# Performance work log

Hardware: AMD Instinct MI355X
Metric: run time of the kernel (lower is better)

## Reference

```python
import jax, jax.numpy as jnp
import numpy as np
import math
from jax import lax

IMG = 1024
STRIDES = (4, 8, 16, 32, 64)
RATIOS = (0.5, 1.0, 2.0)
PRE_NMS = 1000      # pre_nms_top_n['testing'] per level
POST_NMS = 1000     # post_nms_top_n['testing']
NMS_T = 0.7
MIN_SIZE = 1e-3
SCORE_T = 0.0
BBOX_CLAMP = math.log(1000.0 / 16.0)  # torchvision BoxCoder clamp
LEVEL_SIZES = tuple(((IMG // s) ** 2) * len(RATIOS) for s in STRIDES)  # (196608,49152,12288,3072,768)
A_TOTAL = sum(LEVEL_SIZES)
N_IMG = 16


def _make_anchors():
    ratios = np.asarray(RATIOS, dtype=np.float64)
    h_r = np.sqrt(ratios)
    w_r = 1.0 / h_r
    out = []
    for lvl, s in enumerate(STRIDES):
        size = 32.0 * (2 ** lvl)
        ws, hs = w_r * size, h_r * size
        base = np.stack([-ws / 2, -hs / 2, ws / 2, hs / 2], axis=1)  # [A,4]
        g = IMG // s
        coords = np.arange(g, dtype=np.float64) * s
        sx, sy = np.meshgrid(coords, coords)  # [g,g], row = H
        shifts = np.stack([sx, sy, sx, sy], axis=-1).reshape(-1, 1, 4)  # [g*g,1,4] in (H,W,A) order
        out.append((shifts + base[None]).reshape(-1, 4))
    return np.concatenate(out, 0).astype(np.float32)


def setup_inputs() -> dict:
    key = jax.random.key(0)
    k1, k2 = jax.random.split(key)
    objectness = jax.random.normal(k1, (N_IMG, A_TOTAL), dtype=jnp.float32)
    deltas = jax.random.normal(k2, (N_IMG, A_TOTAL, 4), dtype=jnp.float32) * 0.1
    anchors = jnp.asarray(_make_anchors())
    return {"objectness": objectness, "deltas": deltas, "anchors": anchors}


def _decode(deltas, anchors):
    # torchvision BoxCoder.decode with weights (1,1,1,1); deltas [N,A,4], anchors [A,4]
    wa = anchors[:, 2] - anchors[:, 0]
    ha = anchors[:, 3] - anchors[:, 1]
    cxa = anchors[:, 0] + 0.5 * wa
    cya = anchors[:, 1] + 0.5 * ha
    dx, dy, dw, dh = (deltas[..., 0], deltas[..., 1], deltas[..., 2], deltas[..., 3])
    dw = jnp.minimum(dw, BBOX_CLAMP)
    dh = jnp.minimum(dh, BBOX_CLAMP)
    cx = dx * wa + cxa
    cy = dy * ha + cya
    w = jnp.exp(dw) * wa
    h = jnp.exp(dh) * ha
    return jnp.stack([cx - 0.5 * w, cy - 0.5 * h, cx + 0.5 * w, cy + 0.5 * h], axis=-1)


def _nms_image(boxes, scores, lvl, valid):
    # batched_nms via per-level coordinate offset, then greedy NMS over score-sorted boxes.
    max_c = jnp.max(boxes)
    off = lvl.astype(boxes.dtype) * (max_c + 1.0)
    b_off = boxes + off[:, None]
    s = jnp.where(valid, scores, -1.0)
    order = jnp.argsort(-s)
    b = b_off[order]          # [K,4] offset boxes, score-descending
    bo = boxes[order]
    so = scores[order]
    vo = valid[order]
    K = b.shape[0]
    areas = (b[:, 2] - b[:, 0]) * (b[:, 3] - b[:, 1])
    idx = jnp.arange(K)

    def body(keep, xs):
        i, bi, vi = xs
        lt = jnp.maximum(bi[:2], b[:, :2])
        rb = jnp.minimum(bi[2:], b[:, 2:])
        wh = jnp.clip(rb - lt, 0.0)
        inter = wh[:, 0] * wh[:, 1]
        ai = (bi[2] - bi[0]) * (bi[3] - bi[1])
        union = ai + areas - inter
        iou = jnp.where(union > 0, inter / union, 0.0)
        suppressed = jnp.any(keep & (idx < i) & (iou > NMS_T))
        return keep.at[i].set(vi & ~suppressed), None

    keep, _ = lax.scan(body, jnp.zeros((K,), bool), (idx, b, vo))
    # compact kept entries (already score-ordered) into POST_NMS slots, pad with zeros
    pos = jnp.cumsum(keep) - 1
    slot = jnp.where(keep & (pos < POST_NMS), pos, POST_NMS)
    out_b = jnp.zeros((POST_NMS + 1, 4), boxes.dtype).at[slot].set(bo)[:POST_NMS]
    out_s = jnp.zeros((POST_NMS + 1,), boxes.dtype).at[slot].set(so)[:POST_NMS]
    return out_b, out_s


def reference(objectness, deltas, anchors):
    N = objectness.shape[0]
    proposals = _decode(deltas, anchors)  # [N,A,4]
    # per-level top-k (pre-NMS)
    idxs = []
    offset = 0
    for n in LEVEL_SIZES:
        k = min(PRE_NMS, n)
        _, ti = lax.top_k(objectness[:, offset:offset + n], k)
        idxs.append(ti + offset)
        offset += n
    top_idx = jnp.concatenate(idxs, axis=1)  # [N,K]
    obj = jnp.take_along_axis(objectness, top_idx, axis=1)
    props = jnp.take_along_axis(proposals, top_idx[..., None], axis=1)
    lvl_full = jnp.asarray(np.repeat(np.arange(len(LEVEL_SIZES)), LEVEL_SIZES))
    lvl = lvl_full[top_idx]
    scores = jax.nn.sigmoid(obj)
    # clip to image
    x = jnp.clip(props[..., 0::2], 0.0, float(IMG))
    y = jnp.clip(props[..., 1::2], 0.0, float(IMG))
    boxes = jnp.stack([x[..., 0], y[..., 0], x[..., 1], y[..., 1]], axis=-1)
    # remove small boxes + score threshold (as validity mask)
    w = boxes[..., 2] - boxes[..., 0]
    h = boxes[..., 3] - boxes[..., 1]
    valid = (w >= MIN_SIZE) & (h >= MIN_SIZE) & (scores >= SCORE_T)
    out_boxes, out_scores = jax.vmap(_nms_image)(boxes, scores, lvl, valid)
    return out_boxes, out_scores
```

## Files before the change

kernel.cpp:

```cpp
#include <hip/hip_runtime.h>
#include <stdint.h>

#define NIMG 16
#define ATOT 261888
#define TOTC 4768
#define POSTN 1000
#define ROWQ 75
#define EQCAP 8192
#define SCAP 1088
#define BPRE 24
#define DM 0.7000000178813934326171875

__device__ __forceinline__ unsigned sortable_u32(float f) {
  unsigned b = __float_as_uint(f);
  return (b & 0x80000000u) ? ~b : (b | 0x80000000u);
}

__device__ __forceinline__ float exp_xla(float x) {
  float xc = fminf(x, 88.72283935546875f);
  xc = fmaxf(xc, -87.33654022216796875f);
  float n = floorf(fmaf(xc, 1.44269504088896341f, 0.5f));
  float r = fmaf(n, -0.693359375f, xc);
  r = fmaf(n, 2.12194440e-4f, r);
  float y = 1.9875691500e-4f;
  y = fmaf(y, r, 1.3981999507e-3f);
  y = fmaf(y, r, 8.3334519073e-3f);
  y = fmaf(y, r, 4.1665795894e-2f);
  y = fmaf(y, r, 1.6666665459e-1f);
  y = fmaf(y, r, 5.0000001201e-1f);
  float r2 = r * r;
  y = fmaf(y, r2, r);
  y = y + 1.0f;
  return ldexpf(y, (int)n);
}

__device__ __forceinline__ float sigmoid_ref(float x) {
#pragma clang fp contract(off)
  float e = exp_xla(-x);
  return 1.0f / (1.0f + e);
}

__device__ __forceinline__ void chunk_map4k(int c, int& lvl, int& start, int& cnt) {
  if (c < 48)      { lvl = 0; start = c * 4096;        cnt = 4096; }
  else if (c < 60) { lvl = 1; start = (c - 48) * 4096; cnt = 4096; }
  else if (c < 63) { lvl = 2; start = (c - 60) * 4096; cnt = 4096; }
  else             { lvl = 3; start = 0;               cnt = 3072; }
}
__constant__ int d_LO[5] = {0, 196608, 245760, 258048, 261120};
__constant__ int d_CO[5] = {0, 1000, 2000, 3000, 4000};

__global__ void __launch_bounds__(256) k_hist(const float* __restrict__ obj,
                                              unsigned* __restrict__ hist) {
  int img = blockIdx.x >> 6, c = blockIdx.x & 63;
  int lvl, start, cnt;
  chunk_map4k(c, lvl, start, cnt);
  const float4* p4 = (const float4*)(obj + (size_t)img * ATOT + d_LO[lvl] + start);
  __shared__ unsigned h[256];
  h[threadIdx.x] = 0;
  __syncthreads();
  int nv = cnt >> 2;
  for (int i = threadIdx.x; i < nv; i += 256) {
    float4 v = p4[i];
    atomicAdd(&h[sortable_u32(v.x) >> 24], 1u);
    atomicAdd(&h[sortable_u32(v.y) >> 24], 1u);
    atomicAdd(&h[sortable_u32(v.z) >> 24], 1u);
    atomicAdd(&h[sortable_u32(v.w) >> 24], 1u);
  }
  __syncthreads();
  unsigned* gh = hist + (img * 4 + lvl) * 256;
  if (h[threadIdx.x]) atomicAdd(&gh[threadIdx.x], h[threadIdx.x]);
}

__global__ void __launch_bounds__(64) k_thresh(const unsigned* __restrict__ hist,
                                               unsigned* __restrict__ thr) {
  int il = blockIdx.x;
  if (threadIdx.x != 0) return;
  const unsigned* h = hist + il * 256;
  unsigned krem = 1000, cum = 0;
  int d = 255;
  for (; d > 0; --d) {
    if (cum + h[d] >= krem) break;
    cum += h[d];
  }
  thr[il * 2] = (unsigned)d;
  thr[il * 2 + 1] = krem - cum;
}

__global__ void __launch_bounds__(256) k_emit(const float* __restrict__ obj,
                                              const unsigned* __restrict__ thr,
                                              int* __restrict__ cand,
                                              int* __restrict__ eqbuf,
                                              unsigned* __restrict__ cnt) {
  int img = blockIdx.x / 65, c = blockIdx.x % 65;
  if (c == 64) {
    for (int i = threadIdx.x; i < 768; i += 256)
      cand[img * TOTC + d_CO[4] + i] = d_LO[4] + i;
    return;
  }
  int lvl, start, cntn;
  chunk_map4k(c, lvl, start, cntn);
  int il = img * 4 + lvl;
  unsigned d0 = thr[il * 2];
  int gbase = d_LO[lvl] + start;
  const float4* p4 = (const float4*)(obj + (size_t)img * ATOT + gbase);
  int nv = cntn >> 2;
  int cbase = img * TOTC + d_CO[lvl];

  __shared__ int gts[SCAP], eqs[SCAP];
  __shared__ int nGt, nEq, gtBase, eqBase;
  if (threadIdx.x == 0) { nGt = 0; nEq = 0; }
  __syncthreads();

  float4 v[4];
  int ni = 0;
#pragma unroll
  for (int k = 0; k < 4; ++k) {
    int i = threadIdx.x + k * 256;
    if (i < nv) { v[k] = p4[i]; ni = k + 1; }
  }
#pragma unroll
  for (int k = 0; k < 4; ++k) {
    if (k >= ni) break;
    float vv[4] = {v[k].x, v[k].y, v[k].z, v[k].w};
#pragma unroll
    for (int c4 = 0; c4 < 4; ++c4) {
      unsigned u = sortable_u32(vv[c4]);
      unsigned d = u >> 24;
      if (d >= d0) {
        int gidx = gbase + (threadIdx.x + k * 256) * 4 + c4;
        if (d > d0) {
          int p = atomicAdd(&nGt, 1);
          if (p < SCAP) gts[p] = gidx;
          else { int s = (int)atomicAdd(&cnt[il * 2], 1u); cand[cbase + s] = gidx; }
        } else {
          int p = atomicAdd(&nEq, 1);
          if (p < SCAP) eqs[p] = gidx;
          else { int e = (int)atomicAdd(&cnt[il * 2 + 1], 1u); if (e < EQCAP) eqbuf[il * EQCAP + e] = gidx; }
        }
      }
    }
  }
  __syncthreads();
  int ng = nGt < SCAP ? nGt : SCAP;
  int ne = nEq < SCAP ? nEq : SCAP;
  if (threadIdx.x == 0) {
    gtBase = (int)atomicAdd(&cnt[il * 2], (unsigned)ng);
    eqBase = (int)atomicAdd(&cnt[il * 2 + 1], (unsigned)ne);
  }
  __syncthreads();
  for (int k = threadIdx.x; k < ng; k += 256) cand[cbase + gtBase + k] = gts[k];
  for (int k = threadIdx.x; k < ne; k += 256) {
    int e = eqBase + k;
    if (e < EQCAP) eqbuf[il * EQCAP + e] = eqs[k];
  }
}

__global__ void __launch_bounds__(256) k_refine(const float* __restrict__ obj,
                                                const unsigned* __restrict__ thr,
                                                const int* __restrict__ eqbuf,
                                                const unsigned* __restrict__ cnt,
                                                int* __restrict__ cand) {
  int il = blockIdx.x;
  int img = il >> 2, lvl = il & 3;
  unsigned pref = thr[il * 2];
  unsigned krem = thr[il * 2 + 1];
  int neq = min((int)cnt[il * 2 + 1], EQCAP);
  int cgt = (int)cnt[il * 2];
  const float* p = obj + (size_t)img * ATOT;
  const int* eq = eqbuf + il * EQCAP;
  int cbase = img * TOTC + d_CO[lvl];
  __shared__ unsigned h[256];
  __shared__ unsigned s_pref, s_krem;
  for (int round = 1; round < 4; ++round) {
    int shift = 24 - 8 * round;
    h[threadIdx.x] = 0;
    __syncthreads();
    for (int e = threadIdx.x; e < neq; e += 256) {
      unsigned u = sortable_u32(p[eq[e]]);
      if ((u >> (shift + 8)) == pref) atomicAdd(&h[(u >> shift) & 255u], 1u);
    }
    __syncthreads();
    if (threadIdx.x == 0) {
      unsigned cum = 0;
      int d = 255;
      for (; d > 0; --d) {
        if (cum + h[d] >= krem) break;
        cum += h[d];
      }
      s_pref = (pref << 8) | (unsigned)d;
      s_krem = krem - cum;
    }
    __syncthreads();
    pref = s_pref;
    krem = s_krem;
    __syncthreads();
  }
  __shared__ int cg2, ce2;
  __shared__ int eqi[1024];
  if (threadIdx.x == 0) { cg2 = 0; ce2 = 0; }
  __syncthreads();
  for (int e = threadIdx.x; e < neq; e += 256) {
    int gidx = eq[e];
    unsigned u = sortable_u32(p[gidx]);
    if (u > pref) {
      int s = atomicAdd(&cg2, 1);
      cand[cbase + cgt + s] = gidx;
    } else if (u == pref) {
      int s2 = atomicAdd(&ce2, 1);
      if (s2 < 1024) eqi[s2] = gidx;
    }
  }
  __syncthreads();
  if (threadIdx.x == 0) {
    int ne = ce2 < 1024 ? ce2 : 1024;
    int base = cgt + cg2;
    for (int r = 0; r < (int)krem; ++r) {
      int besti = -1, bestv = 0x7fffffff;
      for (int e2 = 0; e2 < ne; ++e2) {
        int v = eqi[e2];
        if (v >= 0 && v < bestv) { bestv = v; besti = e2; }
      }
      if (besti < 0) break;
      eqi[besti] = -1;
      cand[cbase + base + r] = bestv;
    }
  }
}

__global__ void __launch_bounds__(1024) k_lvlsort(const float* __restrict__ obj,
                                                  int* __restrict__ cand) {
  const int KL[5] = {1000, 1000, 1000, 1000, 768};
  const int CO[5] = {0, 1000, 2000, 3000, 4000};
  int img = blockIdx.x / 5, lvl = blockIdx.x % 5;
  int k = KL[lvl];
  int cbase = img * TOTC + CO[lvl];
  int tid = threadIdx.x;
  __shared__ unsigned long long sh[1024];
  unsigned long long key = 0ull;
  if (tid < k) {
    int idx = cand[cbase + tid];
    unsigned u = sortable_u32(obj[(size_t)img * ATOT + idx]);
    key = ((unsigned long long)u << 32) | (unsigned)(0xFFFFFFFFu - (unsigned)idx);
  }
  sh[tid] = key;
  __syncthreads();
  for (int kk = 2; kk <= 1024; kk <<= 1)
    for (int j = kk >> 1; j > 0; j >>= 1) {
      int ixj = tid ^ j;
      if (ixj > tid) {
        unsigned long long a = sh[tid], b = sh[ixj];
        bool up2 = ((tid & kk) == 0);
        if ((a < b) == up2) { sh[tid] = b; sh[ixj] = a; }
      }
      __syncthreads();
    }
  if (tid < k) {
    unsigned low = (unsigned)(sh[tid] & 0xFFFFFFFFull);
    cand[cbase + tid] = (int)(0xFFFFFFFFu - low);
  }
}

__global__ void __launch_bounds__(256) k_decode(const float* __restrict__ obj,
                                                const float* __restrict__ del,
                                                const float* __restrict__ anc,
                                                const int* __restrict__ cand,
                                                float* __restrict__ boxo,
                                                float* __restrict__ keyf,
                                                unsigned* __restrict__ skey,
                                                unsigned* __restrict__ maxcb) {
#pragma clang fp contract(off)
  int img = blockIdx.x;
  int c = blockIdx.y * 256 + threadIdx.x;
  float m = 0.0f;
  if (c < TOTC) {
    int a = cand[img * TOTC + c];
    float o = obj[(size_t)img * ATOT + a];
    float s = sigmoid_ref(o);
    const float* ap = anc + (size_t)a * 4;
    float a0 = ap[0], a1 = ap[1], a2 = ap[2], a3 = ap[3];
    const float* dp = del + ((size_t)img * ATOT + (size_t)a) * 4;
    float dx = dp[0], dy = dp[1], dw = dp[2], dh = dp[3];
    float wa = a2 - a0, ha = a3 - a1;
    float cxa = a0 + 0.5f * wa, cya = a1 + 0.5f * ha;
    dw = fminf(dw, 4.135166556742356f);
    dh = fminf(dh, 4.135166556742356f);
    float cx = dx * wa + cxa;
    float cy = dy * ha + cya;
    float w = exp_xla(dw) * wa;
    float h = exp_xla(dh) * ha;
    float x1 = cx - 0.5f * w, y1 = cy - 0.5f * h;
    float x2 = cx + 0.5f * w, y2 = cy + 0.5f * h;
    x1 = fminf(fmaxf(x1, 0.0f), 1024.0f);
    x2 = fminf(fmaxf(x2, 0.0f), 1024.0f);
    y1 = fminf(fmaxf(y1, 0.0f), 1024.0f);
    y2 = fminf(fmaxf(y2, 0.0f), 1024.0f);
    float ww = x2 - x1, hh = y2 - y1;
    bool valid = (ww >= 1e-3f) && (hh >= 1e-3f) && (s >= 0.0f);
    float kf = valid ? s : -1.0f;
    float4 bx = make_float4(x1, y1, x2, y2);
    *(float4*)(boxo + (size_t)(img * TOTC + c) * 4) = bx;
    keyf[img * TOTC + c] = kf;
    skey[img * TOTC + c] = sortable_u32(kf);
    m = fmaxf(fmaxf(x1, x2), fmaxf(y1, y2));
  }
  __shared__ float red[256];
  red[threadIdx.x] = m;
  __syncthreads();
  for (int s2 = 128; s2 > 0; s2 >>= 1) {
    if (threadIdx.x < s2) red[threadIdx.x] = fmaxf(red[threadIdx.x], red[threadIdx.x + s2]);
    __syncthreads();
  }
  if (threadIdx.x == 0) atomicMax(&maxcb[img], __float_as_uint(red[0]));
}

__global__ void __launch_bounds__(1024) k_gsort(const unsigned* __restrict__ skey,
                                                int* __restrict__ ord) {
  int img = blockIdx.x;
  int tid = threadIdx.x;
  __shared__ unsigned long long sh[8192];
  for (int i = tid; i < 8192; i += 1024) {
    unsigned long long key = 0ull;
    if (i < TOTC) {
      unsigned u = skey[img * TOTC + i];
      key = ((unsigned long long)u << 32) | (unsigned)(0xFFFFu - i);
    }
    sh[i] = key;
  }
  __syncthreads();
  for (int kk = 2; kk <= 8192; kk <<= 1)
    for (int j = kk >> 1; j > 0; j >>= 1) {
      for (int e = tid; e < 8192; e += 1024) {
        int ixj = e ^ j;
        if (ixj > e) {
          unsigned long long a = sh[e], b = sh[ixj];
          bool up2 = ((e & kk) == 0);
          if ((a < b) == up2) { sh[e] = b; sh[ixj] = a; }
        }
      }
      __syncthreads();
    }
  for (int i = tid; i < TOTC; i += 1024) {
    unsigned low = (unsigned)(sh[i] & 0xFFFFull);
    ord[img * TOTC + i] = (int)(0xFFFFu - low);
  }
}

__global__ void __launch_bounds__(256) k_srec(const float* __restrict__ boxo,
                                              const float* __restrict__ keyf,
                                              const int* __restrict__ ord,
                                              const unsigned* __restrict__ maxcb,
                                              float* __restrict__ srec,
                                              int* __restrict__ rinv,
                                              unsigned long long* __restrict__ validw) {
#pragma clang fp contract(off)
  int img = blockIdx.x;
  int i = blockIdx.y * 256 + threadIdx.x;
  if (i >= TOTC) return;
  int p = ord[img * TOTC + i];
  int lvl = p / 1000;
  if (lvl > 4) lvl = 4;
  float4 b = *(const float4*)(boxo + (size_t)(img * TOTC + p) * 4);
  float maxc = __uint_as_float(maxcb[img]);
  float off = (float)lvl * (maxc + 1.0f);
  float ox1 = b.x + off, oy1 = b.y + off, ox2 = b.z + off, oy2 = b.w + off;
  float area = (ox2 - ox1) * (oy2 - oy1);
  float kf = keyf[img * TOTC + p];
  float* r = srec + (size_t)(img * TOTC + i) * 12;
  r[0] = ox1; r[1] = oy1; r[2] = ox2; r[3] = oy2;
  r[4] = area; r[5] = kf;
  r[6] = b.x; r[7] = b.y; r[8] = b.z; r[9] = b.w;
  r[10] = __int_as_float(lvl); r[11] = 0.0f;
  rinv[img * TOTC + p] = i;
  bool valid = kf > -0.5f;
  unsigned long long vb = __ballot(valid);
  if ((threadIdx.x & 63) == 0 && (i >> 6) < ROWQ) validw[img * ROWQ + (i >> 6)] = vb;
}

__global__ void __launch_bounds__(256) k_iou(const float* __restrict__ srec,
                                             unsigned long long* __restrict__ mat) {
#pragma clang fp contract(off)
  int gb = blockIdx.x;
  int img = gb / 21;
  int g = gb % 21;
  int t, jcg;
  if (g < 6)       { t = 0; jcg = g; }
  else if (g < 11) { t = 1; jcg = g - 6; }
  else if (g < 15) { t = 2; jcg = g - 11; }
  else if (g < 18) { t = 3; jcg = g - 15; }
  else if (g < 20) { t = 4; jcg = g - 18; }
  else             { t = 5; jcg = g - 20; }
  int jcbase = (t + jcg) * 4;

  const int tid = threadIdx.x;
  const int i = t * 256 + tid;
  const float* sb = srec + (size_t)img * TOTC * 12;

  __shared__ float4 s_box[256];
  __shared__ float s_area[256];
  {
    int j = jcbase * 64 + tid;
    const float* r = sb + (size_t)j * 12;
    s_box[tid] = *(const float4*)r;
    s_area[tid] = r[4];
  }

  const float* rr = sb + (size_t)i * 12;
  float4 bb = *(const float4*)rr;
  float ix1 = bb.x, iy1 = bb.y, ix2 = bb.z, iy2 = bb.w;
  float ia = rr[4];
  __syncthreads();

  unsigned long long* rowp = mat + ((size_t)img * TOTC + (size_t)i) * ROWQ;
#pragma unroll
  for (int kk = 0; kk < 4; ++kk) {
    int jc = jcbase + kk;
    unsigned long long bits = 0ull;
    for (int b = 0; b < 64; ++b) {
      float4 jb = s_box[kk * 64 + b];
      float ja = s_area[kk * 64 + b];
      float ltx = fmaxf(ix1, jb.x), lty = fmaxf(iy1, jb.y);
      float rbx = fminf(ix2, jb.z), rby = fminf(iy2, jb.w);
      float w = fmaxf(rbx - ltx, 0.0f), h = fmaxf(rby - lty, 0.0f);
      float inter = w * h;
      float uni = (ia + ja) - inter;
      bool sup = (uni > 0.0f) && ((double)inter >= DM * (double)uni);
      if (sup) bits |= (1ull << b);
    }
    rowp[jc] = bits;
  }
}

__global__ void __launch_bounds__(256) k_resolve(const unsigned long long* __restrict__ mat,
                                                 const unsigned long long* __restrict__ validw,
                                                 const float* __restrict__ srec,
                                                 float* __restrict__ out) {
  const int img = blockIdx.x;
  const int tid = threadIdx.x;
  const int lane = tid & 63;
  const int wid = tid >> 6;
  const unsigned long long* matb = mat + (size_t)img * TOTC * ROWQ;
  const float* sb = srec + (size_t)img * TOTC * 12;
  float* ob = out + (size_t)img * POSTN * 4;
  float* os = out + (size_t)NIMG * POSTN * 4 + (size_t)img * POSTN;

  __shared__ int alist[1088];
  __shared__ unsigned long long vw[BPRE];
  __shared__ unsigned long long part[2][4];
  __shared__ unsigned long long sh_keep;
  __shared__ int sh_nacc;
  __shared__ float kb[POSTN][5];

  for (int t = tid; t < BPRE; t += 256) vw[t] = validw[img * ROWQ + t];

  unsigned long long s0 = 0ull;
  int nacc = 0;

  unsigned long long diagcur = 0ull;
  if (wid == 0) diagcur = matb[(size_t)lane * ROWQ + 0];
  __syncthreads();

  for (int B = 0; B < BPRE; ++B) {
    if (lane == B) part[B & 1][wid] = s0;
    __syncthreads();

    unsigned long long supB = part[B & 1][0] | part[B & 1][1] | part[B & 1][2] | part[B & 1][3];
    unsigned long long alive = vw[B] & ~supB;
    const int ibase = B * 64;

    int ri[16];
    unsigned long long rlo[16];
    {
      unsigned long long m = alive;
      for (int t = 0; t < wid; ++t) if (m) m &= m - 1ull;
#pragma unroll
      for (int k = 0; k < 16; ++k) {
        int idx = -1;
        if (m) {
          idx = ibase + __builtin_ctzll(m);
          m &= m - 1ull;
          if (m) m &= m - 1ull;
          if (m) m &= m - 1ull;
          if (m) m &= m - 1ull;
        }
        ri[k] = idx;
        rlo[k] = 0ull;
        if (idx >= 0 && lane < BPRE) rlo[k] = matb[(size_t)idx * ROWQ + lane];
      }
    }

    unsigned long long diagnext = 0ull;
    if (wid == 0) {
      int ibn = (B + 1) * 64 + lane;
      if (B + 1 < BPRE) diagnext = matb[(size_t)ibn * ROWQ + (B + 1)];
      bool alv = ((alive >> lane) & 1ull) != 0ull;
      unsigned long long rem = alive, keepm = 0ull;
      while (rem) {
        int b = __builtin_ctzll(rem);
        keepm |= (1ull << b);
        bool sup = ((diagcur >> b) & 1ull) != 0ull;
        alv = alv && !sup;
        unsigned long long nb = __ballot(alv);
        rem = (b < 63) ? (nb & (~0ull << (b + 1))) : 0ull;
      }
      if (lane == 0) sh_keep = keepm;
      if ((keepm >> lane) & 1ull) {
        int pos = nacc + __popcll(keepm & ((1ull << lane) - 1ull));
        alist[pos] = ibase + lane;
      }
    }
    __syncthreads();
    unsigned long long keepm = sh_keep;
    nacc += __popcll(keepm);
    if (nacc >= POSTN) break;

#pragma unroll
    for (int k = 0; k < 16; ++k) {
      if (ri[k] >= 0 && ((keepm >> (ri[k] - ibase)) & 1ull)) s0 |= rlo[k];
    }
    if (wid == 0) diagcur = diagnext;
  }

  if (nacc < POSTN) {
    for (int k = tid; k < nacc; k += 256) {
      const float* rec = sb + (size_t)alist[k] * 12;
      kb[k][0] = rec[0]; kb[k][1] = rec[1]; kb[k][2] = rec[2]; kb[k][3] = rec[3]; kb[k][4] = rec[4];
    }
    __syncthreads();
    if (wid == 0) {
      int n = nacc;
      for (int r = BPRE * 64; r < TOTC && n < POSTN; ++r) {
        const float* rec = sb + (size_t)r * 12;
        float4 bx = *(const float4*)rec;
        float ra = rec[4];
        float kf = rec[5];
        bool sup = false;
        for (int j = lane; j < n; j += 64) {
          float ltx = fmaxf(bx.x, kb[j][0]), lty = fmaxf(bx.y, kb[j][1]);
          float rbx = fminf(bx.z, kb[j][2]), rby = fminf(bx.w, kb[j][3]);
          float w = fmaxf(rbx - ltx, 0.0f), h = fmaxf(rby - lty, 0.0f);
          float inter = w * h;
          float uni = (ra + kb[j][4]) - inter;
          if (uni > 0.0f && (double)inter >= DM * (double)uni) sup = true;
        }
        bool any = (__ballot(sup) != 0ull);
        if (kf > -0.5f && !any) {
          if (lane == 0) {
            alist[n] = r;
            kb[n][0] = bx.x; kb[n][1] = bx.y; kb[n][2] = bx.z; kb[n][3] = bx.w; kb[n][4] = ra;
          }
          asm volatile("s_waitcnt lgkmcnt(0)" ::: "memory");
          ++n;
        }
      }
      if (lane == 0) sh_nacc = n;
    }
    __syncthreads();
    nacc = sh_nacc;
  }

  __syncthreads();
  int nout = nacc < POSTN ? nacc : POSTN;
  for (int k = tid; k < nout; k += 256) {
    int i = alist[k];
    const float* rec = sb + (size_t)i * 12;
    ob[(size_t)k * 4 + 0] = rec[6];
    ob[(size_t)k * 4 + 1] = rec[7];
    ob[(size_t)k * 4 + 2] = rec[8];
    ob[(size_t)k * 4 + 3] = rec[9];
    os[k] = rec[5];
  }
}

extern "C" void kernel_launch(void* const* d_in, const int* in_sizes, int n_in,
                              void* d_out, int out_size, void* d_ws, size_t ws_size,
                              hipStream_t stream) {
  const float* obj = (const float*)d_in[0];
  const float* del = (const float*)d_in[1];
  const float* anc = (const float*)d_in[2];
  float* out = (float*)d_out;

  char* w = (char*)d_ws;
  size_t o = 0;
  auto carve = [&](size_t bytes) -> char* {
    char* p = w + o;
    o = (o + bytes + 255) & ~(size_t)255;
    return p;
  };
  int* cand = (int*)carve((size_t)NIMG * TOTC * 4);
  unsigned* skey = (unsigned*)carve((size_t)NIMG * TOTC * 4);
  float* keyf = (float*)carve((size_t)NIMG * TOTC * 4);
  int* ord = (int*)carve((size_t)NIMG * TOTC * 4);
  int* rinv = (int*)carve((size_t)NIMG * TOTC * 4);
  float* boxo = (float*)carve((size_t)NIMG * TOTC * 16);
  float* srec = (float*)carve((size_t)NIMG * TOTC * 48);
  unsigned* maxcb = (unsigned*)carve(64);
  unsigned* hist = (unsigned*)carve((size_t)64 * 256 * 4);
  unsigned* thr = (unsigned*)carve((size_t)64 * 2 * 4);
  unsigned* cnt = (unsigned*)carve((size_t)64 * 2 * 4);
  int* eqbuf = (int*)carve((size_t)64 * EQCAP * 4);
  unsigned long long* validw = (unsigned long long*)carve((size_t)NIMG * ROWQ * 8);
  unsigned long long* mat = (unsigned long long*)carve((size_t)NIMG * TOTC * ROWQ * 8);

  hipMemsetAsync(d_out, 0, (size_t)out_size * sizeof(float), stream);
  hipMemsetAsync(maxcb, 0, 16 * sizeof(unsigned), stream);
  hipMemsetAsync(hist, 0, (size_t)64 * 256 * 4, stream);
  hipMemsetAsync(cnt, 0, (size_t)64 * 2 * 4, stream);

  k_hist<<<16 * 64, 256, 0, stream>>>(obj, hist);
  k_thresh<<<64, 64, 0, stream>>>(hist, thr);
  k_emit<<<16 * 65, 256, 0, stream>>>(obj, thr, cand, eqbuf, cnt);
  k_refine<<<64, 256, 0, stream>>>(obj, thr, eqbuf, cnt, cand);
  k_lvlsort<<<80, 1024, 0, stream>>>(obj, cand);
  k_decode<<<dim3(16, (TOTC + 255) / 256), 256, 0, stream>>>(obj, del, anc, cand, boxo, keyf, skey, maxcb);
  k_gsort<<<16, 1024, 0, stream>>>(skey, ord);
  k_srec<<<dim3(16, (TOTC + 255) / 256), 256, 0, stream>>>(boxo, keyf, ord, maxcb, srec, rinv, validw);
  k_iou<<<16 * 21, 256, 0, stream>>>(srec, mat);
  k_resolve<<<16, 256, 0, stream>>>(mat, validw, srec, out);
}
```

Measured before the change: 375.6 us.

## Replace per-image bitonic sort with parallel rank-by-counting across many blocks

Swaps the single-block-per-image 8192-element bitonic sort in shared memory for a counting-rank kernel. Each of 19 tiles per image loads all keys into shared memory, and every thread counts how many keys exceed its own to find its output position. This spreads the work over 304 blocks instead of 16, so more of the GPU is used and the long chain of barriers disappears. In exchange it does O(n²) comparisons, about 4768 per element, and each block reloads the full key array. Keys are now shifted by 16 bits instead of 32; since the index fits in 16 bits, the combined keys stay unique.

```diff
diff --git a/kernel.cpp b/kernel.cpp
--- a/kernel.cpp
+++ b/kernel.cpp
@@ -313,36 +313,26 @@
   if (threadIdx.x == 0) atomicMax(&maxcb[img], __float_as_uint(red[0]));
 }
 
-__global__ void __launch_bounds__(1024) k_gsort(const unsigned* __restrict__ skey,
-                                                int* __restrict__ ord) {
-  int img = blockIdx.x;
-  int tid = threadIdx.x;
-  __shared__ unsigned long long sh[8192];
-  for (int i = tid; i < 8192; i += 1024) {
-    unsigned long long key = 0ull;
-    if (i < TOTC) {
-      unsigned u = skey[img * TOTC + i];
-      key = ((unsigned long long)u << 32) | (unsigned)(0xFFFFu - i);
-    }
-    sh[i] = key;
-  }
-  __syncthreads();
-  for (int kk = 2; kk <= 8192; kk <<= 1)
-    for (int j = kk >> 1; j > 0; j >>= 1) {
-      for (int e = tid; e < 8192; e += 1024) {
-        int ixj = e ^ j;
-        if (ixj > e) {
-          unsigned long long a = sh[e], b = sh[ixj];
-          bool up2 = ((e & kk) == 0);
-          if ((a < b) == up2) { sh[e] = b; sh[ixj] = a; }
-        }
-      }
-      __syncthreads();
-    }
-  for (int i = tid; i < TOTC; i += 1024) {
-    unsigned low = (unsigned)(sh[i] & 0xFFFFull);
-    ord[img * TOTC + i] = (int)(0xFFFFu - low);
-  }
+__global__ void __launch_bounds__(256) k_rank(const unsigned* __restrict__ skey,
+                                              int* __restrict__ ord) {
+  int img = blockIdx.x / 19;
+  int tile = blockIdx.x % 19;
+  __shared__ unsigned long long keys[TOTC];
+  const unsigned* sk = skey + img * TOTC;
+  for (int k = threadIdx.x; k < TOTC; k += 256)
+    keys[k] = ((unsigned long long)sk[k] << 16) | (unsigned)(0xFFFF - k);
+  __syncthreads();
+  int i = tile * 256 + threadIdx.x;
+  if (i >= TOTC) return;
+  unsigned long long my = keys[i];
+  int cnt = 0;
+  int j = 0;
+  for (; j + 8 <= TOTC; j += 8) {
+#pragma unroll
+    for (int u = 0; u < 8; ++u) cnt += (keys[j + u] > my) ? 1 : 0;
+  }
+  for (; j < TOTC; ++j) cnt += (keys[j] > my) ? 1 : 0;
+  ord[img * TOTC + cnt] = i;
 }
 
 __global__ void __launch_bounds__(256) k_srec(const float* __restrict__ boxo,
@@ -612,7 +602,7 @@
   k_refine<<<64, 256, 0, stream>>>(obj, thr, eqbuf, cnt, cand);
   k_lvlsort<<<80, 1024, 0, stream>>>(obj, cand);
   k_decode<<<dim3(16, (TOTC + 255) / 256), 256, 0, stream>>>(obj, del, anc, cand, boxo, keyf, skey, maxcb);
-  k_gsort<<<16, 1024, 0, stream>>>(skey, ord);
+  k_rank<<<16 * 19, 256, 0, stream>>>(skey, ord);
   k_srec<<<dim3(16, (TOTC + 255) / 256), 256, 0, stream>>>(boxo, keyf, ord, maxcb, srec, rinv, validw);
   k_iou<<<16 * 21, 256, 0, stream>>>(srec, mat);
   k_resolve<<<16, 256, 0, stream>>>(mat, validw, srec, out);
```

Result: faster. 331.3 us (-11.8%).
